# Optimization experiments

Measured on AMD Instinct MI355X. Metric: run time of the kernel, lower is better.

## Reference

```python
import jax, jax.numpy as jnp
from jax import lax
import numpy as np

# init kwargs baked as constants (module hyperparameters)
T_LOW = 0.8
T_HIGH = 0.92
Z_RADIUS = 1
XY_RADIUS = 0
DUST_MIN_SIZE = 20


def _shifted(x, axis, step, fill):
    """Shift x by `step` along `axis`, filling vacated slots with `fill`."""
    pad = [(0, 0)] * x.ndim
    n = x.shape[axis]
    if step > 0:
        pad[axis] = (step, 0)
        xp = jnp.pad(x, pad, constant_values=fill)
        return lax.slice_in_dim(xp, 0, n, axis=axis)
    else:
        pad[axis] = (0, -step)
        xp = jnp.pad(x, pad, constant_values=fill)
        return lax.slice_in_dim(xp, -step, n - step, axis=axis)


def _dilate6(m):
    """Binary dilation with 6-connectivity (3D cross incl. center) on [B,D,H,W] bool."""
    out = m
    for ax in (1, 2, 3):
        out = out | _shifted(m, ax, 1, False) | _shifted(m, ax, -1, False)
    return out


def _neighbor_min6(l, big):
    """Min over 6-neighborhood (and self) of int labels; out-of-bounds = big."""
    out = l
    for ax in (1, 2, 3):
        out = jnp.minimum(out, jnp.minimum(_shifted(l, ax, 1, big), _shifted(l, ax, -1, big)))
    return out


def _postprocess(x):
    B, D, H, W = x.shape
    N = D * H * W

    # ---- hysteresis thresholding: grow strong seeds through weak mask ----
    weak = x >= T_LOW
    strong = x >= T_HIGH

    def h_cond(c):
        return c[1]

    def h_body(c):
        m, _ = c
        new = weak & _dilate6(m)
        return new, jnp.any(new != m)

    mask, _ = lax.while_loop(h_cond, h_body, (strong, jnp.array(True)))

    # ---- anisotropic closing: box SE (2*z_r+1, 2*xy_r+1, 2*xy_r+1) ----
    # dilation = max-pool (outside = background), erosion = min-pool (outside = foreground,
    # matching skimage's border_value=1 for erosion so borders are not eaten away)
    win = (1, 2 * Z_RADIUS + 1, 2 * XY_RADIUS + 1, 2 * XY_RADIUS + 1)
    ones = (1, 1, 1, 1)
    mf = mask.astype(jnp.float32)
    dil = lax.reduce_window(mf, -jnp.inf, lax.max, win, ones, 'SAME')
    ero = lax.reduce_window(dil, jnp.inf, lax.min, win, ones, 'SAME')
    mask = ero > 0.5

    # ---- remove_small_objects: CCL via min-label propagation (6-connectivity) ----
    big = jnp.int32(N)  # background sentinel
    flat_ids = jnp.arange(N, dtype=jnp.int32).reshape(1, D, H, W)
    init = jnp.where(mask, flat_ids, big)

    def c_cond(c):
        return c[1]

    def c_body(c):
        lab, _ = c
        new = jnp.where(mask, _neighbor_min6(lab, big), big)
        return new, jnp.any(new != lab)

    labels, _ = lax.while_loop(c_cond, c_body, (init, jnp.array(True)))

    labf = labels.reshape(B, N)
    wf = mask.reshape(B, N).astype(jnp.int32)
    counts = jax.vmap(lambda l, w: jax.ops.segment_sum(w, l, num_segments=N + 1))(labf, wf)
    sizes = jnp.take_along_axis(counts, labf, axis=1).reshape(B, D, H, W)
    keep = mask & (sizes >= DUST_MIN_SIZE)

    # original writes uint8 0/1 back into a float result tensor
    return keep.astype(jnp.float32)


def setup_inputs() -> dict:
    key = jax.random.key(0)
    outputs = jax.random.uniform(key, (8, 16, 384, 384), dtype=jnp.float32)
    return {"outputs": outputs}


def reference(outputs) -> jnp.ndarray:
    return _postprocess(outputs)
```

## Files before the change

### kernel.cpp

```cpp
#include <hip/hip_runtime.h>
#include <stdint.h>

#define B_ 8
#define D_ 16
#define H_ 384
#define W_ 384
constexpr int HW   = H_ * W_;
constexpr int DHW  = D_ * HW;
constexpr int NCOL = B_ * HW;
constexpr unsigned NRUN = (unsigned)NCOL * 8u;

constexpr float T_LOW  = 0.8f;
constexpr float T_HIGH = 0.92f;
constexpr unsigned DUST_MIN = 20u;
constexpr unsigned FLAGGED = 0xFFFFFFFEu;

constexpr int NBLK_QUAD = NCOL / 1024;

constexpr int PTW = 32, PTH = 8;
constexpr int PWB = W_ / PTW;
constexpr int PHB = H_ / PTH;
constexpr int NPATCH = B_ * PWB * PHB;

constexpr int WPAIR_B = (PWB - 1) * H_;
constexpr int HPAIR_B = (PHB - 1) * W_;
constexpr int PAIR_B  = WPAIR_B + HPAIR_B;
constexpr int NPAIRS  = B_ * PAIR_B;

__device__ __forceinline__ unsigned gfind(unsigned* A, unsigned x) {
    for (;;) {
        unsigned p = A[x];
        if (p >= NRUN) return x;
        unsigned g = A[p];
        if (g >= NRUN) return p;
        A[x] = g;
        x = g;
    }
}

__device__ __forceinline__ unsigned groot_val(unsigned* A, unsigned x) {
    for (;;) {
        unsigned p = A[x];
        if (p >= NRUN) return p;
        unsigned g = A[p];
        if (g >= NRUN) return g;
        A[x] = g;
        x = g;
    }
}

__device__ __forceinline__ void set_flag(unsigned* A, unsigned x) {
    unsigned r = gfind(A, x);
    for (;;) {
        unsigned old = atomicMin(&A[r], FLAGGED);
        if (old >= NRUN) return;
        r = gfind(A, old);
    }
}

__device__ __forceinline__ void add_count(unsigned* A, unsigned x, unsigned cnt) {
    unsigned r = gfind(A, x);
    for (;;) {
        unsigned old = A[r];
        if (old < NRUN) { r = gfind(A, old); continue; }
        if (atomicCAS(&A[r], old, old - cnt) == old) return;
    }
}

__device__ __forceinline__ void gunite_flag(unsigned* A, unsigned a, unsigned b) {
    for (;;) {
        a = gfind(A, a);
        b = gfind(A, b);
        if (a == b) return;
        unsigned lo = a < b ? a : b;
        unsigned hi = a < b ? b : a;
        unsigned old = atomicMin(&A[hi], lo);
        if (old >= NRUN) {
            if (old == FLAGGED) set_flag(A, lo);
            return;
        }
        a = lo; b = old;
    }
}

__device__ __forceinline__ void gunite_cnt(unsigned* A, unsigned a, unsigned b) {
    for (;;) {
        a = gfind(A, a);
        b = gfind(A, b);
        if (a == b) return;
        unsigned lo = a < b ? a : b;
        unsigned hi = a < b ? b : a;
        unsigned old = atomicMin(&A[hi], lo);
        if (old >= NRUN) {
            unsigned cnt = 0xFFFFFFFFu - old;
            if (cnt) add_count(A, lo, cnt);
            return;
        }
        a = lo; b = old;
    }
}

__device__ __forceinline__ int runidx(unsigned m, int p) {
    unsigned starts = m & ~(m << 1);
    return __popc(starts & ((2u << p) - 1u)) - 1;
}

__device__ __forceinline__ int nruns(unsigned m) {
    return __popc(m & ~(m << 1));
}

__device__ __forceinline__ unsigned luf_find(unsigned* su, unsigned x) {
    unsigned p = su[x];
    while (p != x) { x = p; p = su[x]; }
    return x;
}

__device__ __forceinline__ void luf_union(unsigned* su, unsigned a, unsigned b) {
    for (;;) {
        a = luf_find(su, a);
        b = luf_find(su, b);
        if (a == b) return;
        unsigned lo = a < b ? a : b;
        unsigned hi = a < b ? b : a;
        unsigned old = atomicMin(&su[hi], lo);
        if (old == hi) return;
        a = lo; b = old;
    }
}

__device__ __forceinline__ void patch_unions(unsigned* su, const unsigned* sm,
                                             unsigned m, int t) {
    int lw = t & 31, lh = t >> 5;
    if (!m) return;
    if (lw < 31) {
        unsigned mB = sm[t + 1];
        unsigned ov = m & mB;
        while (ov) {
            int p = __ffs(ov) - 1;
            luf_union(su, (unsigned)runidx(m, p) * 256 + t,
                          (unsigned)runidx(mB, p) * 256 + t + 1);
            ov &= ov + (1u << p);
        }
    }
    if (lh < 7) {
        unsigned mB = sm[t + 32];
        unsigned ov = m & mB;
        while (ov) {
            int p = __ffs(ov) - 1;
            luf_union(su, (unsigned)runidx(m, p) * 256 + t,
                          (unsigned)runidx(mB, p) * 256 + t + 32);
            ov &= ov + (1u << p);
        }
    }
}


__global__ __launch_bounds__(256) void k_cols(const float* __restrict__ x,
                                              unsigned* __restrict__ cols) {
    int q = blockIdx.x * 256 + threadIdx.x;
    int c0 = q * 4;
    int b = c0 / HW, off = c0 - b * HW;
    const float* xp = x + (size_t)b * DHW + off;
    unsigned wk[4] = {0, 0, 0, 0}, st[4] = {0, 0, 0, 0};
    #pragma unroll
    for (int z = 0; z < D_; ++z) {
        float4 v = *(const float4*)(xp + (size_t)z * HW);
        wk[0] |= (v.x >= T_LOW  ? 1u : 0u) << z;  st[0] |= (v.x >= T_HIGH ? 1u : 0u) << z;
        wk[1] |= (v.y >= T_LOW  ? 1u : 0u) << z;  st[1] |= (v.y >= T_HIGH ? 1u : 0u) << z;
        wk[2] |= (v.z >= T_LOW  ? 1u : 0u) << z;  st[2] |= (v.z >= T_HIGH ? 1u : 0u) << z;
        wk[3] |= (v.w >= T_LOW  ? 1u : 0u) << z;  st[3] |= (v.w >= T_HIGH ? 1u : 0u) << z;
    }
    *(uint4*)(cols + c0) = make_uint4(wk[0] | (st[0] << 16), wk[1] | (st[1] << 16),
                                      wk[2] | (st[2] << 16), wk[3] | (st[3] << 16));
}

__global__ __launch_bounds__(256) void k_loc1(const unsigned* __restrict__ cols,
                                              unsigned* __restrict__ parent1) {
    __shared__ unsigned sm[256];
    __shared__ unsigned su[2048];
    __shared__ unsigned sf[2048];
    int blk = blockIdx.x;
    int b = blk / (PHB * PWB), pr = blk % (PHB * PWB);
    int h0 = (pr / PWB) * PTH, w0 = (pr % PWB) * PTW;
    int t = threadIdx.x;
    int c = b * HW + (h0 + (t >> 5)) * W_ + (w0 + (t & 31));
    unsigned cc = cols[c];
    unsigned m = cc & 0xFFFFu, st = cc >> 16;
    sm[t] = m;
    #pragma unroll
    for (int i = 0; i < 8; ++i) { su[i * 256 + t] = i * 256 + t; sf[i * 256 + t] = 0; }
    __syncthreads();
    patch_unions(su, sm, m, t);
    __syncthreads();
    if (st) {
        unsigned rem = m; int idx = 0;
        while (rem) {
            int p = __ffs(rem) - 1;
            unsigned tt = rem >> p;
            int len = __ffs(~tt) - 1;
            unsigned runmask = ((1u << len) - 1u) << p;
            if (runmask & st) sf[luf_find(su, (unsigned)idx * 256 + t)] = 1u;
            rem &= ~runmask; ++idx;
        }
    }
    __syncthreads();
    int nr = nruns(m);
    for (int i = 0; i < nr; ++i) {
        unsigned lid = (unsigned)i * 256 + t;
        unsigned lr  = luf_find(su, lid);
        unsigned gid = (unsigned)i * NCOL + c;
        if (lr == lid) parent1[gid] = sf[lid] ? FLAGGED : 0xFFFFFFFFu;
        else {
            unsigned tt = lr & 255u, ss = lr >> 8;
            parent1[gid] = ss * NCOL +
                (unsigned)(b * HW + (h0 + (int)(tt >> 5)) * W_ + (w0 + (int)(tt & 31)));
        }
    }
}

__global__ __launch_bounds__(256) void k_bnd1(const unsigned* __restrict__ cols,
                                              unsigned* parent1) {
    int e = blockIdx.x * 256 + threadIdx.x;
    if (e >= NPAIRS) return;
    int b = e / PAIR_B, r = e % PAIR_B;
    int cA, cB;
    if (r < WPAIR_B) {
        int h = r / (PWB - 1), wi = r % (PWB - 1);
        cA = b * HW + h * W_ + wi * PTW + (PTW - 1);
        cB = cA + 1;
    } else {
        r -= WPAIR_B;
        int hi = r / W_, w = r % W_;
        cA = b * HW + (hi * PTH + (PTH - 1)) * W_ + w;
        cB = cA + W_;
    }
    unsigned mA = cols[cA] & 0xFFFFu;
    unsigned mB = cols[cB] & 0xFFFFu;
    unsigned ov = mA & mB;
    while (ov) {
        int p = __ffs(ov) - 1;
        gunite_flag(parent1, (unsigned)runidx(mA, p) * NCOL + cA,
                             (unsigned)runidx(mB, p) * NCOL + cB);
        ov &= ov + (1u << p);
    }
}

__global__ __launch_bounds__(256) void k_loc2(const unsigned* __restrict__ cols,
                                              unsigned* parent1,
                                              unsigned short* __restrict__ closed,
                                              unsigned* __restrict__ parent2) {
    __shared__ unsigned sm[256];
    __shared__ unsigned su[2048];
    __shared__ unsigned sc[2048];
    int blk = blockIdx.x;
    int b = blk / (PHB * PWB), pr = blk % (PHB * PWB);
    int h0 = (pr / PWB) * PTH, w0 = (pr % PWB) * PTW;
    int t = threadIdx.x;
    int c = b * HW + (h0 + (t >> 5)) * W_ + (w0 + (t & 31));
    unsigned wk = cols[c] & 0xFFFFu;
    unsigned m = 0;
    {
        unsigned rem = wk; int idx = 0;
        while (rem) {
            int p = __ffs(rem) - 1;
            unsigned tt = rem >> p;
            int len = __ffs(~tt) - 1;
            unsigned runmask = ((1u << len) - 1u) << p;
            if (groot_val(parent1, (unsigned)idx * NCOL + c) == FLAGGED)
                m |= runmask;
            rem &= ~runmask; ++idx;
        }
    }
    unsigned dil = (m | (m << 1) | (m >> 1)) & 0xFFFFu;
    unsigned ero = dil & ((dil << 1) | 1u) & ((dil >> 1) | 0x8000u);
    closed[c] = (unsigned short)ero;

    sm[t] = ero;
    #pragma unroll
    for (int i = 0; i < 8; ++i) { su[i * 256 + t] = i * 256 + t; sc[i * 256 + t] = 0; }
    __syncthreads();
    patch_unions(su, sm, ero, t);
    __syncthreads();
    {
        unsigned rem = ero; int idx = 0;
        while (rem) {
            int p = __ffs(rem) - 1;
            unsigned tt = rem >> p;
            int len = __ffs(~tt) - 1;
            unsigned runmask = ((1u << len) - 1u) << p;
            atomicAdd(&sc[luf_find(su, (unsigned)idx * 256 + t)], (unsigned)len);
            rem &= ~runmask; ++idx;
        }
    }
    __syncthreads();
    int nr = nruns(ero);
    for (int i = 0; i < nr; ++i) {
        unsigned lid = (unsigned)i * 256 + t;
        unsigned lr  = luf_find(su, lid);
        unsigned gid = (unsigned)i * NCOL + c;
        if (lr == lid) parent2[gid] = 0xFFFFFFFFu - sc[lid];
        else {
            unsigned tt = lr & 255u, ss = lr >> 8;
            parent2[gid] = ss * NCOL +
                (unsigned)(b * HW + (h0 + (int)(tt >> 5)) * W_ + (w0 + (int)(tt & 31)));
        }
    }
}

__global__ __launch_bounds__(256) void k_bnd2(const unsigned short* __restrict__ closed,
                                              unsigned* parent2) {
    int e = blockIdx.x * 256 + threadIdx.x;
    if (e >= NPAIRS) return;
    int b = e / PAIR_B, r = e % PAIR_B;
    int cA, cB;
    if (r < WPAIR_B) {
        int h = r / (PWB - 1), wi = r % (PWB - 1);
        cA = b * HW + h * W_ + wi * PTW + (PTW - 1);
        cB = cA + 1;
    } else {
        r -= WPAIR_B;
        int hi = r / W_, w = r % W_;
        cA = b * HW + (hi * PTH + (PTH - 1)) * W_ + w;
        cB = cA + W_;
    }
    unsigned mA = closed[cA];
    unsigned mB = closed[cB];
    unsigned ov = mA & mB;
    while (ov) {
        int p = __ffs(ov) - 1;
        gunite_cnt(parent2, (unsigned)runidx(mA, p) * NCOL + cA,
                            (unsigned)runidx(mB, p) * NCOL + cB);
        ov &= ov + (1u << p);
    }
}

__global__ __launch_bounds__(256) void k_out(const unsigned short* __restrict__ closed,
                                             unsigned* parent2,
                                             float* __restrict__ out) {
    int q = blockIdx.x * 256 + threadIdx.x;
    int c0 = q * 4;
    int b = c0 / HW, off = c0 - b * HW;
    unsigned keep[4];
    #pragma unroll
    for (int j = 0; j < 4; ++j) {
        int c = c0 + j;
        unsigned fg = closed[c];
        unsigned k = 0;
        unsigned rem = fg; int idx = 0;
        while (rem) {
            int p = __ffs(rem) - 1;
            unsigned tt = rem >> p;
            int len = __ffs(~tt) - 1;
            unsigned runmask = ((1u << len) - 1u) << p;
            if (0xFFFFFFFFu - groot_val(parent2, (unsigned)idx * NCOL + c) >= DUST_MIN)
                k |= runmask;
            rem &= ~runmask; ++idx;
        }
        keep[j] = k;
    }
    float* op = out + (size_t)b * DHW + off;
    #pragma unroll
    for (int z = 0; z < D_; ++z) {
        *(float4*)(op + (size_t)z * HW) =
            make_float4((keep[0] >> z) & 1u ? 1.0f : 0.0f,
                        (keep[1] >> z) & 1u ? 1.0f : 0.0f,
                        (keep[2] >> z) & 1u ? 1.0f : 0.0f,
                        (keep[3] >> z) & 1u ? 1.0f : 0.0f);
    }
}

extern "C" void kernel_launch(void* const* d_in, const int* in_sizes, int n_in,
                              void* d_out, int out_size, void* d_ws, size_t ws_size,
                              hipStream_t stream) {
    const float* x = (const float*)d_in[0];
    float* out = (float*)d_out;

    const size_t sz_parent = (size_t)NRUN * 4;
    const size_t sz_cols   = (size_t)NCOL * 4;
    const size_t sz_closed = (size_t)NCOL * 2;
    if (ws_size < 2 * sz_parent + sz_cols + sz_closed) return;
    char* ws = (char*)d_ws;
    unsigned*       parent1 = (unsigned*)ws;
    unsigned*       parent2 = (unsigned*)(ws + sz_parent);
    unsigned*       cols    = (unsigned*)(ws + 2 * sz_parent);
    unsigned short* closed  = (unsigned short*)(ws + 2 * sz_parent + sz_cols);

    dim3 blk(256);
    dim3 grdQ(NBLK_QUAD), grdL(NPATCH), grdB((NPAIRS + 255) / 256);

    k_cols<<<grdQ, blk, 0, stream>>>(x, cols);
    k_loc1<<<grdL, blk, 0, stream>>>(cols, parent1);
    k_bnd1<<<grdB, blk, 0, stream>>>(cols, parent1);

    k_loc2<<<grdL, blk, 0, stream>>>(cols, parent1, closed, parent2);
    k_bnd2<<<grdB, blk, 0, stream>>>(closed, parent2);
    k_out<<<grdQ, blk, 0, stream>>>(closed, parent2, out);
}
```

Baseline: 278.6 us.

## Fuse thresholding into local CCL kernel, shrink mask, prefetch parent chains

The column-threshold kernel is removed and its work moved into the first patch-local labeling kernel, which reads the input floats directly and writes a 16-bit weak mask instead of a 32-bit packed column word. The shared-memory find now does path halving. The second local kernel and the output kernel prefetch the first few parent entries for each column into registers before walking the union-find chains, so those loads can overlap. This removes one launch and one intermediate round trip through memory, at the cost of scalar instead of float4 input loads and more registers per thread.

Measured after the change: 258.5 us. -7.2%, faster.

```diff
diff --git a/kernel.cpp b/kernel.cpp
--- a/kernel.cpp
+++ b/kernel.cpp
@@ -110,9 +110,14 @@
 }
 
 __device__ __forceinline__ unsigned luf_find(unsigned* su, unsigned x) {
-    unsigned p = su[x];
-    while (p != x) { x = p; p = su[x]; }
-    return x;
+    for (;;) {
+        unsigned p = su[x];
+        if (p == x) return x;
+        unsigned g = su[p];
+        if (g == p) return p;
+        su[x] = g;
+        x = g;
+    }
 }
 
 __device__ __forceinline__ void luf_union(unsigned* su, unsigned a, unsigned b) {
@@ -155,26 +160,8 @@
 }
 
 
-__global__ __launch_bounds__(256) void k_cols(const float* __restrict__ x,
-                                              unsigned* __restrict__ cols) {
-    int q = blockIdx.x * 256 + threadIdx.x;
-    int c0 = q * 4;
-    int b = c0 / HW, off = c0 - b * HW;
-    const float* xp = x + (size_t)b * DHW + off;
-    unsigned wk[4] = {0, 0, 0, 0}, st[4] = {0, 0, 0, 0};
-    #pragma unroll
-    for (int z = 0; z < D_; ++z) {
-        float4 v = *(const float4*)(xp + (size_t)z * HW);
-        wk[0] |= (v.x >= T_LOW  ? 1u : 0u) << z;  st[0] |= (v.x >= T_HIGH ? 1u : 0u) << z;
-        wk[1] |= (v.y >= T_LOW  ? 1u : 0u) << z;  st[1] |= (v.y >= T_HIGH ? 1u : 0u) << z;
-        wk[2] |= (v.z >= T_LOW  ? 1u : 0u) << z;  st[2] |= (v.z >= T_HIGH ? 1u : 0u) << z;
-        wk[3] |= (v.w >= T_LOW  ? 1u : 0u) << z;  st[3] |= (v.w >= T_HIGH ? 1u : 0u) << z;
-    }
-    *(uint4*)(cols + c0) = make_uint4(wk[0] | (st[0] << 16), wk[1] | (st[1] << 16),
-                                      wk[2] | (st[2] << 16), wk[3] | (st[3] << 16));
-}
-
-__global__ __launch_bounds__(256) void k_loc1(const unsigned* __restrict__ cols,
+__global__ __launch_bounds__(256) void k_loc1(const float* __restrict__ x,
+                                              unsigned short* __restrict__ weakm,
                                               unsigned* __restrict__ parent1) {
     __shared__ unsigned sm[256];
     __shared__ unsigned su[2048];
@@ -184,8 +171,17 @@
     int h0 = (pr / PWB) * PTH, w0 = (pr % PWB) * PTW;
     int t = threadIdx.x;
     int c = b * HW + (h0 + (t >> 5)) * W_ + (w0 + (t & 31));
-    unsigned cc = cols[c];
-    unsigned m = cc & 0xFFFFu, st = cc >> 16;
+    const float* xp = x + (size_t)b * DHW + (size_t)(h0 + (t >> 5)) * W_ + (w0 + (t & 31));
+    float vz[16];
+    #pragma unroll
+    for (int z = 0; z < 16; ++z) vz[z] = xp[(size_t)z * HW];
+    unsigned m = 0, st = 0;
+    #pragma unroll
+    for (int z = 0; z < 16; ++z) {
+        m  |= (vz[z] >= T_LOW  ? 1u : 0u) << z;
+        st |= (vz[z] >= T_HIGH ? 1u : 0u) << z;
+    }
+    weakm[c] = (unsigned short)m;
     sm[t] = m;
     #pragma unroll
     for (int i = 0; i < 8; ++i) { su[i * 256 + t] = i * 256 + t; sf[i * 256 + t] = 0; }
@@ -218,7 +214,7 @@
     }
 }
 
-__global__ __launch_bounds__(256) void k_bnd1(const unsigned* __restrict__ cols,
+__global__ __launch_bounds__(256) void k_bnd1(const unsigned short* __restrict__ weakm,
                                               unsigned* parent1) {
     int e = blockIdx.x * 256 + threadIdx.x;
     if (e >= NPAIRS) return;
@@ -234,8 +230,8 @@
         cA = b * HW + (hi * PTH + (PTH - 1)) * W_ + w;
         cB = cA + W_;
     }
-    unsigned mA = cols[cA] & 0xFFFFu;
-    unsigned mB = cols[cB] & 0xFFFFu;
+    unsigned mA = weakm[cA];
+    unsigned mB = weakm[cB];
     unsigned ov = mA & mB;
     while (ov) {
         int p = __ffs(ov) - 1;
@@ -245,7 +241,7 @@
     }
 }
 
-__global__ __launch_bounds__(256) void k_loc2(const unsigned* __restrict__ cols,
+__global__ __launch_bounds__(256) void k_loc2(const unsigned short* __restrict__ weakm,
                                               unsigned* parent1,
                                               unsigned short* __restrict__ closed,
                                               unsigned* __restrict__ parent2) {
@@ -257,7 +253,11 @@
     int h0 = (pr / PWB) * PTH, w0 = (pr % PWB) * PTW;
     int t = threadIdx.x;
     int c = b * HW + (h0 + (t >> 5)) * W_ + (w0 + (t & 31));
-    unsigned wk = cols[c] & 0xFFFFu;
+    unsigned wk = weakm[c];
+    int nrw = nruns(wk);
+    unsigned pv[4];
+    #pragma unroll
+    for (int i = 0; i < 4; ++i) if (i < nrw) pv[i] = parent1[(unsigned)i * NCOL + c];
     unsigned m = 0;
     {
         unsigned rem = wk; int idx = 0;
@@ -266,8 +266,10 @@
             unsigned tt = rem >> p;
             int len = __ffs(~tt) - 1;
             unsigned runmask = ((1u << len) - 1u) << p;
-            if (groot_val(parent1, (unsigned)idx * NCOL + c) == FLAGGED)
-                m |= runmask;
+            unsigned rv;
+            if (idx < 4) { unsigned v = pv[idx]; rv = (v >= NRUN) ? v : groot_val(parent1, v); }
+            else rv = groot_val(parent1, (unsigned)idx * NCOL + c);
+            if (rv == FLAGGED) m |= runmask;
             rem &= ~runmask; ++idx;
         }
     }
@@ -340,20 +342,32 @@
     int q = blockIdx.x * 256 + threadIdx.x;
     int c0 = q * 4;
     int b = c0 / HW, off = c0 - b * HW;
+    ushort4 cc4 = *(const ushort4*)(closed + c0);
+    unsigned fg[4] = {cc4.x, cc4.y, cc4.z, cc4.w};
+    unsigned pv[4][4];
+    int nr[4];
+    #pragma unroll
+    for (int j = 0; j < 4; ++j) {
+        nr[j] = nruns(fg[j]);
+        #pragma unroll
+        for (int i = 0; i < 4; ++i)
+            if (i < nr[j]) pv[j][i] = parent2[(unsigned)i * NCOL + (c0 + j)];
+    }
     unsigned keep[4];
     #pragma unroll
     for (int j = 0; j < 4; ++j) {
         int c = c0 + j;
-        unsigned fg = closed[c];
         unsigned k = 0;
-        unsigned rem = fg; int idx = 0;
+        unsigned rem = fg[j]; int idx = 0;
         while (rem) {
             int p = __ffs(rem) - 1;
             unsigned tt = rem >> p;
             int len = __ffs(~tt) - 1;
             unsigned runmask = ((1u << len) - 1u) << p;
-            if (0xFFFFFFFFu - groot_val(parent2, (unsigned)idx * NCOL + c) >= DUST_MIN)
-                k |= runmask;
+            unsigned rv;
+            if (idx < 4) { unsigned v = pv[j][idx]; rv = (v >= NRUN) ? v : groot_val(parent2, v); }
+            else rv = groot_val(parent2, (unsigned)idx * NCOL + c);
+            if (0xFFFFFFFFu - rv >= DUST_MIN) k |= runmask;
             rem &= ~runmask; ++idx;
         }
         keep[j] = k;
@@ -376,23 +390,21 @@
     float* out = (float*)d_out;
 
     const size_t sz_parent = (size_t)NRUN * 4;
-    const size_t sz_cols   = (size_t)NCOL * 4;
-    const size_t sz_closed = (size_t)NCOL * 2;
-    if (ws_size < 2 * sz_parent + sz_cols + sz_closed) return;
+    const size_t sz_mask   = (size_t)NCOL * 2;
+    if (ws_size < 2 * sz_parent + 2 * sz_mask) return;
     char* ws = (char*)d_ws;
     unsigned*       parent1 = (unsigned*)ws;
     unsigned*       parent2 = (unsigned*)(ws + sz_parent);
-    unsigned*       cols    = (unsigned*)(ws + 2 * sz_parent);
-    unsigned short* closed  = (unsigned short*)(ws + 2 * sz_parent + sz_cols);
+    unsigned short* weakm   = (unsigned short*)(ws + 2 * sz_parent);
+    unsigned short* closed  = (unsigned short*)(ws + 2 * sz_parent + sz_mask);
 
     dim3 blk(256);
-    dim3 grdQ(NBLK_QUAD), grdL(NPATCH), grdB((NPAIRS + 255) / 256);
-
-    k_cols<<<grdQ, blk, 0, stream>>>(x, cols);
-    k_loc1<<<grdL, blk, 0, stream>>>(cols, parent1);
-    k_bnd1<<<grdB, blk, 0, stream>>>(cols, parent1);
-
-    k_loc2<<<grdL, blk, 0, stream>>>(cols, parent1, closed, parent2);
+    dim3 grdL(NPATCH), grdB((NPAIRS + 255) / 256), grdQ(NBLK_QUAD);
+
+    k_loc1<<<grdL, blk, 0, stream>>>(x, weakm, parent1);
+    k_bnd1<<<grdB, blk, 0, stream>>>(weakm, parent1);
+
+    k_loc2<<<grdL, blk, 0, stream>>>(weakm, parent1, closed, parent2);
     k_bnd2<<<grdB, blk, 0, stream>>>(closed, parent2);
     k_out<<<grdQ, blk, 0, stream>>>(closed, parent2, out);
 }
```
